# Kernel tuning notes

Hardware: AMD Instinct MI355X
Metric: run time of the kernel (lower is better)

Reference implementation:

```python
import jax, jax.numpy as jnp
import numpy as np

NUM_CLASSES = 20
NUM_ANCHORS = 3
STRIDES = (8, 16, 32)
FMP = (320, 160, 80)
TOPK = 100
CONF_THRESH = 0.01
NMS_THRESH = 0.5
ANCHOR_SIZE = np.array([[12, 16], [19, 36], [40, 28], [36, 75], [76, 55], [72, 146],
                        [142, 110], [192, 243], [459, 401]], dtype=np.float32).reshape(3, NUM_ANCHORS, 2)


def make_anchors(level):
    h = w = FMP[level]
    ys, xs = jnp.meshgrid(jnp.arange(h, dtype=jnp.float32), jnp.arange(w, dtype=jnp.float32), indexing='ij')
    xy = jnp.stack([xs, ys], axis=-1).reshape(-1, 1, 2) + 0.5            # [HW,1,2] grid centers
    xy = jnp.broadcast_to(xy, (h * w, NUM_ANCHORS, 2))
    wh = jnp.broadcast_to(jnp.asarray(ANCHOR_SIZE[level]), (h * w, NUM_ANCHORS, 2))
    return jnp.concatenate([xy, wh], axis=-1).reshape(-1, 4)             # [HW*A, 4]


def level_topk(obj, cls, reg, level):
    C = NUM_CLASSES
    # [1, ch, H, W] -> [H*W*A, ch_per_anchor], matching permute(1,2,0).view(-1, .)
    obj = obj[0].transpose(1, 2, 0).reshape(-1, 1)
    cls = cls[0].transpose(1, 2, 0).reshape(-1, C)
    reg = reg[0].transpose(1, 2, 0).reshape(-1, 4)
    anchors = make_anchors(level)
    # decode: ctr = (sigmoid(txy)*3 - 1.5 + grid) * stride ; wh = exp(twh) * anchor_wh
    ctr = (jax.nn.sigmoid(reg[:, :2]) * 3.0 - 1.5 + anchors[:, :2]) * STRIDES[level]
    wh = jnp.exp(reg[:, 2:]) * anchors[:, 2:]
    boxes = jnp.concatenate([ctr - 0.5 * wh, ctr + 0.5 * wh], axis=-1)   # [N, 4] xyxy
    scores = (jax.nn.sigmoid(obj) * jax.nn.sigmoid(cls)).reshape(-1)     # [N*C]
    top_s, top_i = jax.lax.top_k(scores, TOPK)
    anchor_idx = top_i // C
    labels = top_i % C
    return top_s, labels, boxes[anchor_idx], top_s > CONF_THRESH


def nms_fixed(boxes, scores, labels, valid):
    # class-aware greedy NMS on a fixed candidate set; suppressed entries get score 0 / keep False
    K = scores.shape[0]
    order = jnp.argsort(-scores)
    b, s, l, v = boxes[order], scores[order], labels[order], valid[order]
    areas = (b[:, 2] - b[:, 0]) * (b[:, 3] - b[:, 1])
    xx1 = jnp.maximum(b[:, None, 0], b[None, :, 0])
    yy1 = jnp.maximum(b[:, None, 1], b[None, :, 1])
    xx2 = jnp.minimum(b[:, None, 2], b[None, :, 2])
    yy2 = jnp.minimum(b[:, None, 3], b[None, :, 3])
    inter = jnp.maximum(1e-10, xx2 - xx1) * jnp.maximum(1e-10, yy2 - yy1)
    iou = inter / (areas[:, None] + areas[None, :] - inter)
    sup_mat = (iou > NMS_THRESH) & (l[:, None] == l[None, :])            # per-class suppression
    idx = jnp.arange(K)

    def body(i, state):
        suppressed, keep = state
        is_kept = jnp.logical_and(jnp.logical_not(suppressed[i]), v[i])
        keep = keep.at[i].set(is_kept)
        suppressed = suppressed | (is_kept & sup_mat[i] & (idx > i))
        return suppressed, keep

    _, keep = jax.lax.fori_loop(0, K, body, (jnp.zeros(K, bool), jnp.zeros(K, bool)))
    return b, s * keep.astype(s.dtype), l, keep


def setup_inputs() -> dict:
    key = jax.random.key(0)
    ks = jax.random.split(key, 9)
    shapes = {
        'obj0': (1, NUM_ANCHORS, 320, 320), 'cls0': (1, NUM_ANCHORS * NUM_CLASSES, 320, 320), 'reg0': (1, NUM_ANCHORS * 4, 320, 320),
        'obj1': (1, NUM_ANCHORS, 160, 160), 'cls1': (1, NUM_ANCHORS * NUM_CLASSES, 160, 160), 'reg1': (1, NUM_ANCHORS * 4, 160, 160),
        'obj2': (1, NUM_ANCHORS, 80, 80), 'cls2': (1, NUM_ANCHORS * NUM_CLASSES, 80, 80), 'reg2': (1, NUM_ANCHORS * 4, 80, 80),
    }
    return {name: jax.random.normal(k, shp, dtype=jnp.float32)
            for k, (name, shp) in zip(ks, shapes.items())}


def reference(obj0, cls0, reg0, obj1, cls1, reg1, obj2, cls2, reg2):
    levels = [(obj0, cls0, reg0), (obj1, cls1, reg1), (obj2, cls2, reg2)]
    parts = [level_topk(o, c, r, i) for i, (o, c, r) in enumerate(levels)]
    scores = jnp.concatenate([p[0] for p in parts])
    labels = jnp.concatenate([p[1] for p in parts])
    boxes = jnp.concatenate([p[2] for p in parts])
    valid = jnp.concatenate([p[3] for p in parts])
    return nms_fixed(boxes, scores, labels, valid)  # (bboxes[300,4], scores[300], labels[300], keep[300])
```

## Files before the change

### kernel.cpp

```cpp
#include <hip/hip_runtime.h>
#include <stdint.h>

typedef unsigned int u32;
typedef unsigned long long u64;

#define TOPK 100
#define CAP 4096
#define NB 512
#define BINBASE 32000u
#define KAB_BLOCKS 394

__device__ const float ANC[3][3][2] = {
  {{12.f,16.f},{19.f,36.f},{40.f,28.f}},
  {{36.f,75.f},{76.f,55.f},{72.f,146.f}},
  {{142.f,110.f},{192.f,243.f},{459.f,401.f}}
};

__device__ __forceinline__ float sigmoidf_(float x) {
  if (x >= 0.f) return 1.f / (1.f + expf(-x));
  float e = expf(x);
  return e / (1.f + e);
}

__device__ __forceinline__ float fcomp(const float4& v, int q) {
  switch (q) {
    case 0: return v.x;
    case 1: return v.y;
    case 2: return v.z;
    default: return v.w;
  }
}

__global__ __launch_bounds__(256) void kA_scan(
    const float* __restrict__ obj0, const float* __restrict__ cls0,
    const float* __restrict__ obj1, const float* __restrict__ cls1,
    const float* __restrict__ obj2, const float* __restrict__ cls2,
    u32* __restrict__ hist, float* __restrict__ amax)
{
  __shared__ u32 h[NB];
  int tid = threadIdx.x;
  h[tid] = 0; h[tid + 256] = 0;
  __syncthreads();

  int b = blockIdx.x;
  const float *obj, *cls; int P, L, abase; u32 task;
  if (b < 300)      { L=0; obj=obj0; cls=cls0; P=102400; abase=0;      task=(u32)(b*256+tid); }
  else if (b < 375) { L=1; obj=obj1; cls=cls1; P=25600;  abase=307200; task=(u32)((b-300)*256+tid); }
  else              { L=2; obj=obj2; cls=cls2; P=6400;   abase=384000; task=(u32)((b-375)*256+tid); }
  int tpa = P >> 2;
  bool valid = task < (u32)(3*tpa);

  if (valid) {
    int a = (int)(task / (u32)tpa), rem = (int)(task % (u32)tpa);
    int p0 = rem * 4;
    float4 o4 = *(const float4*)(obj + a*P + p0);
    const float* cp = cls + (size_t)(a*20)*P + p0;
    float4 cv[20];
    #pragma unroll
    for (int k = 0; k < 20; ++k) cv[k] = *(const float4*)(cp + (size_t)k*P);
    float4 cm = cv[0];
    #pragma unroll
    for (int k = 1; k < 20; ++k) {
      cm.x = fmaxf(cm.x, cv[k].x); cm.y = fmaxf(cm.y, cv[k].y);
      cm.z = fmaxf(cm.z, cv[k].z); cm.w = fmaxf(cm.w, cv[k].w);
    }
    float4 am4;
    am4.x = sigmoidf_(o4.x) * sigmoidf_(cm.x);
    am4.y = sigmoidf_(o4.y) * sigmoidf_(cm.y);
    am4.z = sigmoidf_(o4.z) * sigmoidf_(cm.z);
    am4.w = sigmoidf_(o4.w) * sigmoidf_(cm.w);
    *(float4*)(amax + abase + a*P + p0) = am4;
    #pragma unroll
    for (int q = 0; q < 4; ++q) {
      u32 bt = __float_as_uint(fcomp(am4, q));
      if (bt >= (BINBASE << 15)) {
        u32 bin = (bt >> 15) - BINBASE;
        if (bin < NB) atomicAdd(&h[bin], 1u);
      }
    }
  }
  __syncthreads();
  if (h[tid])       atomicAdd(&hist[L*NB + tid],       h[tid]);
  if (h[tid + 256]) atomicAdd(&hist[L*NB + tid + 256], h[tid + 256]);
}

__global__ __launch_bounds__(256) void kB_collect(
    const float* __restrict__ obj0, const float* __restrict__ cls0,
    const float* __restrict__ obj1, const float* __restrict__ cls1,
    const float* __restrict__ obj2, const float* __restrict__ cls2,
    const float* __restrict__ amax, const u32* __restrict__ hist,
    u32* __restrict__ cnt, u64* __restrict__ cand)
{
  __shared__ u32 s[NB];
  __shared__ u32 sThr;
  int tid = threadIdx.x;
  int b = blockIdx.x;
  const float *obj, *cls; int P, L, abase; u32 task;
  if (b < 300)      { L=0; obj=obj0; cls=cls0; P=102400; abase=0;      task=(u32)(b*256+tid); }
  else if (b < 375) { L=1; obj=obj1; cls=cls1; P=25600;  abase=307200; task=(u32)((b-300)*256+tid); }
  else              { L=2; obj=obj2; cls=cls2; P=6400;   abase=384000; task=(u32)((b-375)*256+tid); }
  int tpa = P >> 2;
  bool valid = task < (u32)(3*tpa);

  s[tid] = hist[L*NB + tid]; s[tid + 256] = hist[L*NB + tid + 256];
  __syncthreads();
  for (int off = 1; off < NB; off <<= 1) {
    u32 v0 = s[tid]       + ((tid + off < NB)       ? s[tid + off]       : 0u);
    u32 v1 = s[tid + 256] + ((tid + 256 + off < NB) ? s[tid + 256 + off] : 0u);
    __syncthreads();
    s[tid] = v0; s[tid + 256] = v1;
    __syncthreads();
  }
  if (tid == 0 && s[0] < TOPK) sThr = BINBASE << 15;
  {
    int i0 = tid, i1 = tid + 256;
    u32 a0 = s[i0], n0 = (i0 + 1 < NB) ? s[i0 + 1] : 0u;
    if (a0 >= TOPK && n0 < TOPK) sThr = (BINBASE + (u32)i0) << 15;
    u32 a1 = s[i1], n1 = (i1 + 1 < NB) ? s[i1 + 1] : 0u;
    if (a1 >= TOPK && n1 < TOPK) sThr = (BINBASE + (u32)i1) << 15;
  }
  __syncthreads();
  u32 thr = sThr;

  if (valid) {
    int a = (int)(task / (u32)tpa), rem = (int)(task % (u32)tpa);
    int p0 = rem * 4;
    float4 am4 = *(const float4*)(amax + abase + a*P + p0);
    bool any = (__float_as_uint(am4.x) >= thr) | (__float_as_uint(am4.y) >= thr) |
               (__float_as_uint(am4.z) >= thr) | (__float_as_uint(am4.w) >= thr);
    if (any) {
      float4 o4 = *(const float4*)(obj + a*P + p0);
      const float* cp = cls + (size_t)(a*20)*P + p0;
      float4 cv[20];
      #pragma unroll
      for (int k = 0; k < 20; ++k) cv[k] = *(const float4*)(cp + (size_t)k*P);
      #pragma unroll
      for (int q = 0; q < 4; ++q) {
        if (__float_as_uint(fcomp(am4, q)) >= thr) {
          float so = sigmoidf_(fcomp(o4, q));
          int p = p0 + q;
          #pragma unroll
          for (int k = 0; k < 20; ++k) {
            float sc = so * sigmoidf_(fcomp(cv[k], q));
            u32 bits = __float_as_uint(sc);
            if (bits >= thr) {
              u32 pos = atomicAdd(&cnt[L], 1u);
              u32 idx = (u32)(p*60 + a*20 + k);
              if (pos < CAP) cand[L*CAP + pos] = ((u64)bits << 32) | (u64)(0x00FFFFFFu - idx);
            }
          }
        }
      }
    }
  }
}

__global__ __launch_bounds__(1024) void kC_select_nms(
    const float* __restrict__ reg0, const float* __restrict__ reg1, const float* __restrict__ reg2,
    const u64* __restrict__ cand, const u32* __restrict__ cnt,
    float* __restrict__ out)
{
  extern __shared__ uint8_t smem[];
  u64*    keys  = (u64*)(smem);
  u64*    mat   = (u64*)(smem);
  float4* ibox4 = (float4*)(smem + 12000);
  float2* iml2  = (float2*)(smem + 16800);
  float*  x1s   = (float*)(smem + 19200);
  float*  y1s   = (float*)(smem + 20400);
  float*  x2s   = (float*)(smem + 21600);
  float*  y2s   = (float*)(smem + 22800);
  float*  sc2   = (float*)(smem + 24000);
  int*    lb2   = (int*)(smem + 25200);
  int*    vd2   = (int*)(smem + 26400);
  u64*    rowAny= (u64*)(smem + 27600);
  u64*    km    = (u64*)(smem + 27648);
  float*  ars   = (float*)(smem + 27696);
  u64*    sel   = (u64*)(smem + 32800);
  float*  bxs   = (float*)(smem + 35200);
  float*  scs   = (float*)(smem + 40000);
  int*    lbs   = (int*)(smem + 41200);
  int*    vds   = (int*)(smem + 42400);

  int tid = threadIdx.x;
  if (tid < 300) sel[tid] = 0ull;
  __syncthreads();

  for (int L = 0; L < 3; ++L) {
    u32 n = cnt[L]; if (n > CAP) n = CAP;
    u32 n4 = (n + 3u) & ~3u;
    for (u32 j = (u32)tid; j < n; j += 1024) keys[j] = cand[L*CAP + j];
    if (tid < 4 && n + (u32)tid < n4) keys[n + tid] = 0ull;
    __syncthreads();
    for (u32 j = (u32)tid; j < n; j += 1024) {
      u64 kk = keys[j]; int r = 0;
      for (u32 t = 0; t < n4; t += 4) {
        u64 k0 = keys[t], k1 = keys[t+1], k2 = keys[t+2], k3 = keys[t+3];
        r += (k0 > kk) ? 1 : 0; r += (k1 > kk) ? 1 : 0;
        r += (k2 > kk) ? 1 : 0; r += (k3 > kk) ? 1 : 0;
      }
      if (r < TOPK) sel[L*TOPK + r] = kk;
    }
    __syncthreads();
  }

  if (tid < 300) {
    int Lq = tid / TOPK;
    const float* reg; int Pq, W, stride;
    if (Lq == 0)      { reg = reg0; Pq = 102400; W = 320; stride = 8; }
    else if (Lq == 1) { reg = reg1; Pq = 25600;  W = 160; stride = 16; }
    else              { reg = reg2; Pq = 6400;   W = 80;  stride = 32; }
    u64 key = sel[tid];
    if (key == 0) {
      scs[tid] = 0.f; lbs[tid] = 0; vds[tid] = 0;
      bxs[tid*4+0] = bxs[tid*4+1] = bxs[tid*4+2] = bxs[tid*4+3] = 0.f;
    } else {
      float score = __uint_as_float((u32)(key >> 32));
      u32 i = 0x00FFFFFFu - (u32)(key & 0xFFFFFFFFull);
      int c = (int)(i % 60u), p = (int)(i / 60u);
      int aa = c / 20, k = c % 20;
      int x = p % W, y = p / W;
      float tx = reg[(aa*4+0)*Pq + p], ty = reg[(aa*4+1)*Pq + p];
      float tw = reg[(aa*4+2)*Pq + p], th = reg[(aa*4+3)*Pq + p];
      float cx = (sigmoidf_(tx)*3.f - 1.5f + (float)x + 0.5f) * (float)stride;
      float cy = (sigmoidf_(ty)*3.f - 1.5f + (float)y + 0.5f) * (float)stride;
      float bw = expf(tw) * ANC[Lq][aa][0];
      float bh = expf(th) * ANC[Lq][aa][1];
      scs[tid] = score; lbs[tid] = k; vds[tid] = (score > 0.01f) ? 1 : 0;
      bxs[tid*4+0] = cx - 0.5f*bw; bxs[tid*4+1] = cy - 0.5f*bh;
      bxs[tid*4+2] = cx + 0.5f*bw; bxs[tid*4+3] = cy + 0.5f*bh;
    }
  }
  __syncthreads();

  if (tid < 300) {
    int Lm = tid / TOPK, rr = tid % TOPK;
    u64 kk = sel[tid];
    int rank = rr;
    #pragma unroll
    for (int Lo = 0; Lo < 3; ++Lo) {
      if (Lo == Lm) continue;
      const u64* arr = sel + Lo*TOPK;
      bool ge = (Lo < Lm);
      int lo = 0;
      #pragma unroll
      for (int st = 64; st > 0; st >>= 1) {
        int nxt = lo + st;
        if (nxt <= TOPK) {
          u64 v = arr[nxt - 1];
          bool pred = ge ? (v >= kk) : (v > kk);
          if (pred) lo = nxt;
        }
      }
      rank += lo;
    }
    float x1 = bxs[tid*4+0], y1 = bxs[tid*4+1], x2 = bxs[tid*4+2], y2 = bxs[tid*4+3];
    float ar = (x2 - x1) * (y2 - y1);
    ibox4[rank] = make_float4(x1, y1, x2, y2);
    iml2[rank]  = make_float2(ar, (float)lbs[tid]);
    x1s[rank] = x1; y1s[rank] = y1; x2s[rank] = x2; y2s[rank] = y2; ars[rank] = ar;
    sc2[rank] = scs[tid]; lb2[rank] = lbs[tid]; vd2[rank] = vds[tid];
  }
  __syncthreads();

  {
    int wave = tid >> 6, lane = tid & 63;
    if (wave < 15) {
      int w = wave / 3, stripe = wave % 3;
      int j = w*64 + lane;
      bool jv = j < 300;
      float jx1=0.f, jy1=0.f, jx2=0.f, jy2=0.f, jar=0.f; float jlb=-1.f;
      if (jv) { jx1=x1s[j]; jy1=y1s[j]; jx2=x2s[j]; jy2=y2s[j]; jar=ars[j]; jlb=(float)lb2[j]; }
      int ilim = (w+1)*64; if (ilim > 300) ilim = 300;
      #pragma unroll 2
      for (int i = stripe; i < ilim; i += 3) {
        float4 B = ibox4[i];
        float2 M = iml2[i];
        float xx1 = fmaxf(B.x, jx1), yy1 = fmaxf(B.y, jy1);
        float xx2 = fminf(B.z, jx2), yy2 = fminf(B.w, jy2);
        float inter = fmaxf(1e-10f, xx2-xx1) * fmaxf(1e-10f, yy2-yy1);
        float iou = inter / (M.x + jar - inter);
        bool pred = jv && (iou > 0.5f) && (M.y == jlb);
        u64 m = __ballot(pred);
        if (lane == 0) mat[i*5 + w] = m;
      }
    }
  }
  __syncthreads();

  {
    bool flag = false;
    if (tid < 300) {
      int c = tid >> 6, bq = tid & 63;
      u64 acc = mat[tid*5 + c] & ((bq == 63) ? 0ull : (~0ull << (bq + 1)));
      for (int w = c + 1; w < 5; ++w) acc |= mat[tid*5 + w];
      flag = (acc != 0ull);
    }
    u64 bal = __ballot(flag);
    if ((tid & 63) == 0 && (tid >> 6) < 5) rowAny[tid >> 6] = bal;
  }
  __syncthreads();

  if (tid < 64) {
    int lane = tid;
    u64 vm[5];
    #pragma unroll
    for (int c = 0; c < 5; ++c) {
      int j = c*64 + lane;
      vm[c] = __ballot((j < 300) && (vd2[j] != 0));
    }
    u64 ra[5];
    #pragma unroll
    for (int c = 0; c < 5; ++c) ra[c] = rowAny[c];
    u64 S[5] = {0,0,0,0,0};
    #pragma unroll
    for (int c = 0; c < 5; ++c) {
      u64 kbits = 0;
      int lim = (c == 4) ? 44 : 64;
      for (int t = 0; t < lim; ++t) {
        u64 kept = ((~(S[c] >> t)) & (vm[c] >> t)) & 1ull;
        kbits |= kept << t;
        if (kept & ((ra[c] >> t) & 1ull)) {
          int i = c*64 + t;
          #pragma unroll
          for (int w = 0; w < 5; ++w)
            if (w >= c) S[w] |= mat[i*5 + w];
        }
      }
      if (lane == 0) km[c] = kbits;
    }
  }
  __syncthreads();

  if (tid < 300) {
    float kf = (float)((km[tid >> 6] >> (tid & 63)) & 1ull);
    float4 bq = ibox4[tid];
    out[tid*4+0] = bq.x; out[tid*4+1] = bq.y;
    out[tid*4+2] = bq.z; out[tid*4+3] = bq.w;
    out[1200+tid] = sc2[tid] * kf;
    out[1500+tid] = (float)lb2[tid];
    out[1800+tid] = kf;
  }
}

extern "C" void kernel_launch(void* const* d_in, const int* in_sizes, int n_in,
                              void* d_out, int out_size, void* d_ws, size_t ws_size,
                              hipStream_t stream) {
  const float* obj0 = (const float*)d_in[0];
  const float* cls0 = (const float*)d_in[1];
  const float* reg0 = (const float*)d_in[2];
  const float* obj1 = (const float*)d_in[3];
  const float* cls1 = (const float*)d_in[4];
  const float* reg1 = (const float*)d_in[5];
  const float* obj2 = (const float*)d_in[6];
  const float* cls2 = (const float*)d_in[7];
  const float* reg2 = (const float*)d_in[8];
  float* out = (float*)d_out;

  uint8_t* ws = (uint8_t*)d_ws;
  u32*   hist = (u32*)(ws + 0);
  u32*   cnt  = (u32*)(ws + 6144);
  u64*   cand = (u64*)(ws + 8192);
  float* amax = (float*)(ws + 106496);

  (void)hipMemsetAsync(ws, 0, 6160, stream);

  kA_scan<<<dim3(KAB_BLOCKS), dim3(256), 0, stream>>>(
      obj0, cls0, obj1, cls1, obj2, cls2, hist, amax);
  kB_collect<<<dim3(KAB_BLOCKS), dim3(256), 0, stream>>>(
      obj0, cls0, obj1, cls1, obj2, cls2, amax, hist, cnt, cand);
  kC_select_nms<<<dim3(1), dim3(1024), 46080, stream>>>(reg0, reg1, reg2, cand, cnt, out);
}
```

Baseline: 165.1 us.

## Split select+NMS kernel into per-level parallel select and separate NMS kernel

The single-block select+NMS kernel is split in two. The first kernel runs one block per pyramid level, doing the rank-based top-100 selection and box decode in parallel across levels and writing the results to workspace. The second kernel merges the levels and runs NMS. The IoU matrix build also changes from a uniform 3 stripes per column wave to a triangular split, giving later column groups more waves. This adds a kernel launch, a global round trip, and workspace reuse of the amax region, which is safe only if amax is dead by then.

```diff
diff --git a/kernel.cpp b/kernel.cpp
--- a/kernel.cpp
+++ b/kernel.cpp
@@ -155,13 +155,73 @@
   }
 }
 
-__global__ __launch_bounds__(1024) void kC_select_nms(
+__global__ __launch_bounds__(256) void kC1_select(
     const float* __restrict__ reg0, const float* __restrict__ reg1, const float* __restrict__ reg2,
     const u64* __restrict__ cand, const u32* __restrict__ cnt,
+    u64* __restrict__ selg, float* __restrict__ boxg, float* __restrict__ scg,
+    int* __restrict__ lbg, int* __restrict__ vdg)
+{
+  __shared__ u64 keys[CAP + 4];
+  __shared__ u64 selL[TOPK];
+  int tid = threadIdx.x;
+  int L = blockIdx.x;
+
+  if (tid < TOPK) selL[tid] = 0ull;
+  __syncthreads();
+
+  u32 n = cnt[L]; if (n > CAP) n = CAP;
+  u32 n4 = (n + 3u) & ~3u;
+  for (u32 j = (u32)tid; j < n; j += 256) keys[j] = cand[L*CAP + j];
+  if (tid < 4 && n + (u32)tid < n4) keys[n + tid] = 0ull;
+  __syncthreads();
+
+  for (u32 j = (u32)tid; j < n; j += 256) {
+    u64 kk = keys[j]; int r = 0;
+    for (u32 t = 0; t < n4; t += 4) {
+      u64 k0 = keys[t], k1 = keys[t+1], k2 = keys[t+2], k3 = keys[t+3];
+      r += (k0 > kk) ? 1 : 0; r += (k1 > kk) ? 1 : 0;
+      r += (k2 > kk) ? 1 : 0; r += (k3 > kk) ? 1 : 0;
+    }
+    if (r < TOPK) selL[r] = kk;
+  }
+  __syncthreads();
+
+  if (tid < TOPK) {
+    const float* reg; int Pq, W, stride;
+    if (L == 0)      { reg = reg0; Pq = 102400; W = 320; stride = 8; }
+    else if (L == 1) { reg = reg1; Pq = 25600;  W = 160; stride = 16; }
+    else             { reg = reg2; Pq = 6400;   W = 80;  stride = 32; }
+    int g = L*TOPK + tid;
+    u64 key = selL[tid];
+    selg[g] = key;
+    if (key == 0) {
+      scg[g] = 0.f; lbg[g] = 0; vdg[g] = 0;
+      boxg[g*4+0] = boxg[g*4+1] = boxg[g*4+2] = boxg[g*4+3] = 0.f;
+    } else {
+      float score = __uint_as_float((u32)(key >> 32));
+      u32 i = 0x00FFFFFFu - (u32)(key & 0xFFFFFFFFull);
+      int c = (int)(i % 60u), p = (int)(i / 60u);
+      int aa = c / 20, k = c % 20;
+      int x = p % W, y = p / W;
+      float tx = reg[(aa*4+0)*Pq + p], ty = reg[(aa*4+1)*Pq + p];
+      float tw = reg[(aa*4+2)*Pq + p], th = reg[(aa*4+3)*Pq + p];
+      float cx = (sigmoidf_(tx)*3.f - 1.5f + (float)x + 0.5f) * (float)stride;
+      float cy = (sigmoidf_(ty)*3.f - 1.5f + (float)y + 0.5f) * (float)stride;
+      float bw = expf(tw) * ANC[L][aa][0];
+      float bh = expf(th) * ANC[L][aa][1];
+      scg[g] = score; lbg[g] = k; vdg[g] = (score > 0.01f) ? 1 : 0;
+      boxg[g*4+0] = cx - 0.5f*bw; boxg[g*4+1] = cy - 0.5f*bh;
+      boxg[g*4+2] = cx + 0.5f*bw; boxg[g*4+3] = cy + 0.5f*bh;
+    }
+  }
+}
+
+__global__ __launch_bounds__(1024) void kC2_nms(
+    const u64* __restrict__ selg, const float* __restrict__ boxg,
+    const float* __restrict__ scg, const int* __restrict__ lbg, const int* __restrict__ vdg,
     float* __restrict__ out)
 {
   extern __shared__ uint8_t smem[];
-  u64*    keys  = (u64*)(smem);
   u64*    mat   = (u64*)(smem);
   float4* ibox4 = (float4*)(smem + 12000);
   float2* iml2  = (float2*)(smem + 16800);
@@ -175,71 +235,20 @@
   u64*    rowAny= (u64*)(smem + 27600);
   u64*    km    = (u64*)(smem + 27648);
   float*  ars   = (float*)(smem + 27696);
-  u64*    sel   = (u64*)(smem + 32800);
-  float*  bxs   = (float*)(smem + 35200);
-  float*  scs   = (float*)(smem + 40000);
-  int*    lbs   = (int*)(smem + 41200);
-  int*    vds   = (int*)(smem + 42400);
+  u64*    selAll= (u64*)(smem + 28896);
 
   int tid = threadIdx.x;
-  if (tid < 300) sel[tid] = 0ull;
-  __syncthreads();
-
-  for (int L = 0; L < 3; ++L) {
-    u32 n = cnt[L]; if (n > CAP) n = CAP;
-    u32 n4 = (n + 3u) & ~3u;
-    for (u32 j = (u32)tid; j < n; j += 1024) keys[j] = cand[L*CAP + j];
-    if (tid < 4 && n + (u32)tid < n4) keys[n + tid] = 0ull;
-    __syncthreads();
-    for (u32 j = (u32)tid; j < n; j += 1024) {
-      u64 kk = keys[j]; int r = 0;
-      for (u32 t = 0; t < n4; t += 4) {
-        u64 k0 = keys[t], k1 = keys[t+1], k2 = keys[t+2], k3 = keys[t+3];
-        r += (k0 > kk) ? 1 : 0; r += (k1 > kk) ? 1 : 0;
-        r += (k2 > kk) ? 1 : 0; r += (k3 > kk) ? 1 : 0;
-      }
-      if (r < TOPK) sel[L*TOPK + r] = kk;
-    }
-    __syncthreads();
-  }
-
-  if (tid < 300) {
-    int Lq = tid / TOPK;
-    const float* reg; int Pq, W, stride;
-    if (Lq == 0)      { reg = reg0; Pq = 102400; W = 320; stride = 8; }
-    else if (Lq == 1) { reg = reg1; Pq = 25600;  W = 160; stride = 16; }
-    else              { reg = reg2; Pq = 6400;   W = 80;  stride = 32; }
-    u64 key = sel[tid];
-    if (key == 0) {
-      scs[tid] = 0.f; lbs[tid] = 0; vds[tid] = 0;
-      bxs[tid*4+0] = bxs[tid*4+1] = bxs[tid*4+2] = bxs[tid*4+3] = 0.f;
-    } else {
-      float score = __uint_as_float((u32)(key >> 32));
-      u32 i = 0x00FFFFFFu - (u32)(key & 0xFFFFFFFFull);
-      int c = (int)(i % 60u), p = (int)(i / 60u);
-      int aa = c / 20, k = c % 20;
-      int x = p % W, y = p / W;
-      float tx = reg[(aa*4+0)*Pq + p], ty = reg[(aa*4+1)*Pq + p];
-      float tw = reg[(aa*4+2)*Pq + p], th = reg[(aa*4+3)*Pq + p];
-      float cx = (sigmoidf_(tx)*3.f - 1.5f + (float)x + 0.5f) * (float)stride;
-      float cy = (sigmoidf_(ty)*3.f - 1.5f + (float)y + 0.5f) * (float)stride;
-      float bw = expf(tw) * ANC[Lq][aa][0];
-      float bh = expf(th) * ANC[Lq][aa][1];
-      scs[tid] = score; lbs[tid] = k; vds[tid] = (score > 0.01f) ? 1 : 0;
-      bxs[tid*4+0] = cx - 0.5f*bw; bxs[tid*4+1] = cy - 0.5f*bh;
-      bxs[tid*4+2] = cx + 0.5f*bw; bxs[tid*4+3] = cy + 0.5f*bh;
-    }
-  }
+  if (tid < 300) selAll[tid] = selg[tid];
   __syncthreads();
 
   if (tid < 300) {
     int Lm = tid / TOPK, rr = tid % TOPK;
-    u64 kk = sel[tid];
+    u64 kk = selAll[tid];
     int rank = rr;
     #pragma unroll
     for (int Lo = 0; Lo < 3; ++Lo) {
       if (Lo == Lm) continue;
-      const u64* arr = sel + Lo*TOPK;
+      const u64* arr = selAll + Lo*TOPK;
       bool ge = (Lo < Lm);
       int lo = 0;
       #pragma unroll
@@ -253,26 +262,29 @@
       }
       rank += lo;
     }
-    float x1 = bxs[tid*4+0], y1 = bxs[tid*4+1], x2 = bxs[tid*4+2], y2 = bxs[tid*4+3];
+    float4 bb = *(const float4*)(boxg + tid*4);
+    float x1 = bb.x, y1 = bb.y, x2 = bb.z, y2 = bb.w;
     float ar = (x2 - x1) * (y2 - y1);
     ibox4[rank] = make_float4(x1, y1, x2, y2);
-    iml2[rank]  = make_float2(ar, (float)lbs[tid]);
+    iml2[rank]  = make_float2(ar, (float)lbg[tid]);
     x1s[rank] = x1; y1s[rank] = y1; x2s[rank] = x2; y2s[rank] = y2; ars[rank] = ar;
-    sc2[rank] = scs[tid]; lb2[rank] = lbs[tid]; vd2[rank] = vds[tid];
+    sc2[rank] = scg[tid]; lb2[rank] = lbg[tid]; vd2[rank] = vdg[tid];
   }
   __syncthreads();
 
   {
     int wave = tid >> 6, lane = tid & 63;
     if (wave < 15) {
-      int w = wave / 3, stripe = wave % 3;
+      int w = (wave >= 10) ? 4 : (wave >= 6) ? 3 : (wave >= 3) ? 2 : (wave >= 1) ? 1 : 0;
+      int ns = w + 1;
+      int stripe = wave - ((w*(w+1)) >> 1);
       int j = w*64 + lane;
       bool jv = j < 300;
       float jx1=0.f, jy1=0.f, jx2=0.f, jy2=0.f, jar=0.f; float jlb=-1.f;
       if (jv) { jx1=x1s[j]; jy1=y1s[j]; jx2=x2s[j]; jy2=y2s[j]; jar=ars[j]; jlb=(float)lb2[j]; }
       int ilim = (w+1)*64; if (ilim > 300) ilim = 300;
       #pragma unroll 2
-      for (int i = stripe; i < ilim; i += 3) {
+      for (int i = stripe; i < ilim; i += ns) {
         float4 B = ibox4[i];
         float2 M = iml2[i];
         float xx1 = fmaxf(B.x, jx1), yy1 = fmaxf(B.y, jy1);
@@ -361,6 +373,11 @@
   u32*   cnt  = (u32*)(ws + 6144);
   u64*   cand = (u64*)(ws + 8192);
   float* amax = (float*)(ws + 106496);
+  u64*   selg = (u64*)(ws + 106496);
+  float* boxg = (float*)(ws + 108896);
+  float* scg  = (float*)(ws + 113696);
+  int*   lbg  = (int*)(ws + 114896);
+  int*   vdg  = (int*)(ws + 116096);
 
   (void)hipMemsetAsync(ws, 0, 6160, stream);
 
@@ -368,5 +385,8 @@
       obj0, cls0, obj1, cls1, obj2, cls2, hist, amax);
   kB_collect<<<dim3(KAB_BLOCKS), dim3(256), 0, stream>>>(
       obj0, cls0, obj1, cls1, obj2, cls2, amax, hist, cnt, cand);
-  kC_select_nms<<<dim3(1), dim3(1024), 46080, stream>>>(reg0, reg1, reg2, cand, cnt, out);
-}
+  kC1_select<<<dim3(3), dim3(256), 0, stream>>>(
+      reg0, reg1, reg2, cand, cnt, selg, boxg, scg, lbg, vdg);
+  kC2_nms<<<dim3(1), dim3(1024), 31744, stream>>>(
+      selg, boxg, scg, lbg, vdg, out);
+}
```

Result: faster. 157.3 us (-4.7%).

## Halve per-thread work in scan kernels, parallelize per-level selection, rebalance IoU waves

Applied to the files above, without the earlier changes.

The scan and collect kernels now process two pixels per thread using float2 loads, which doubles the block count to 788 and raises parallelism and memory-level concurrency across the GPU. The single-block select/NMS kernel now ranks candidates for all three levels at once, each with its own thread group, instead of looping over levels in sequence. Keys are kept in LDS when a level has few candidates, and a global-memory fallback handles larger counts. The IoU matrix waves are split in proportion to the triangular workload per column block, and the shared-memory size is reduced. The costs are narrower loads per thread, fewer threads working on each level's ranking, and a slow global-memory path if a level's candidate count is large.

```diff
diff --git a/kernel.cpp b/kernel.cpp
--- a/kernel.cpp
+++ b/kernel.cpp
@@ -8,7 +8,7 @@
 #define CAP 4096
 #define NB 512
 #define BINBASE 32000u
-#define KAB_BLOCKS 394
+#define KAB_BLOCKS 788
 
 __device__ const float ANC[3][3][2] = {
   {{12.f,16.f},{19.f,36.f},{40.f,28.f}},
@@ -22,13 +22,8 @@
   return e / (1.f + e);
 }
 
-__device__ __forceinline__ float fcomp(const float4& v, int q) {
-  switch (q) {
-    case 0: return v.x;
-    case 1: return v.y;
-    case 2: return v.z;
-    default: return v.w;
-  }
+__device__ __forceinline__ float fcomp2(const float2& v, int q) {
+  return q ? v.y : v.x;
 }
 
 __global__ __launch_bounds__(256) void kA_scan(
@@ -44,35 +39,32 @@
 
   int b = blockIdx.x;
   const float *obj, *cls; int P, L, abase; u32 task;
-  if (b < 300)      { L=0; obj=obj0; cls=cls0; P=102400; abase=0;      task=(u32)(b*256+tid); }
-  else if (b < 375) { L=1; obj=obj1; cls=cls1; P=25600;  abase=307200; task=(u32)((b-300)*256+tid); }
-  else              { L=2; obj=obj2; cls=cls2; P=6400;   abase=384000; task=(u32)((b-375)*256+tid); }
-  int tpa = P >> 2;
+  if (b < 600)      { L=0; obj=obj0; cls=cls0; P=102400; abase=0;      task=(u32)(b*256+tid); }
+  else if (b < 750) { L=1; obj=obj1; cls=cls1; P=25600;  abase=307200; task=(u32)((b-600)*256+tid); }
+  else              { L=2; obj=obj2; cls=cls2; P=6400;   abase=384000; task=(u32)((b-750)*256+tid); }
+  int tpa = P >> 1;
   bool valid = task < (u32)(3*tpa);
 
   if (valid) {
     int a = (int)(task / (u32)tpa), rem = (int)(task % (u32)tpa);
-    int p0 = rem * 4;
-    float4 o4 = *(const float4*)(obj + a*P + p0);
+    int p0 = rem * 2;
+    float2 o2 = *(const float2*)(obj + a*P + p0);
     const float* cp = cls + (size_t)(a*20)*P + p0;
-    float4 cv[20];
-    #pragma unroll
-    for (int k = 0; k < 20; ++k) cv[k] = *(const float4*)(cp + (size_t)k*P);
-    float4 cm = cv[0];
+    float2 cv[20];
+    #pragma unroll
+    for (int k = 0; k < 20; ++k) cv[k] = *(const float2*)(cp + (size_t)k*P);
+    float2 cm = cv[0];
     #pragma unroll
     for (int k = 1; k < 20; ++k) {
       cm.x = fmaxf(cm.x, cv[k].x); cm.y = fmaxf(cm.y, cv[k].y);
-      cm.z = fmaxf(cm.z, cv[k].z); cm.w = fmaxf(cm.w, cv[k].w);
-    }
-    float4 am4;
-    am4.x = sigmoidf_(o4.x) * sigmoidf_(cm.x);
-    am4.y = sigmoidf_(o4.y) * sigmoidf_(cm.y);
-    am4.z = sigmoidf_(o4.z) * sigmoidf_(cm.z);
-    am4.w = sigmoidf_(o4.w) * sigmoidf_(cm.w);
-    *(float4*)(amax + abase + a*P + p0) = am4;
-    #pragma unroll
-    for (int q = 0; q < 4; ++q) {
-      u32 bt = __float_as_uint(fcomp(am4, q));
+    }
+    float2 am2;
+    am2.x = sigmoidf_(o2.x) * sigmoidf_(cm.x);
+    am2.y = sigmoidf_(o2.y) * sigmoidf_(cm.y);
+    *(float2*)(amax + abase + a*P + p0) = am2;
+    #pragma unroll
+    for (int q = 0; q < 2; ++q) {
+      u32 bt = __float_as_uint(fcomp2(am2, q));
       if (bt >= (BINBASE << 15)) {
         u32 bin = (bt >> 15) - BINBASE;
         if (bin < NB) atomicAdd(&h[bin], 1u);
@@ -96,10 +88,10 @@
   int tid = threadIdx.x;
   int b = blockIdx.x;
   const float *obj, *cls; int P, L, abase; u32 task;
-  if (b < 300)      { L=0; obj=obj0; cls=cls0; P=102400; abase=0;      task=(u32)(b*256+tid); }
-  else if (b < 375) { L=1; obj=obj1; cls=cls1; P=25600;  abase=307200; task=(u32)((b-300)*256+tid); }
-  else              { L=2; obj=obj2; cls=cls2; P=6400;   abase=384000; task=(u32)((b-375)*256+tid); }
-  int tpa = P >> 2;
+  if (b < 600)      { L=0; obj=obj0; cls=cls0; P=102400; abase=0;      task=(u32)(b*256+tid); }
+  else if (b < 750) { L=1; obj=obj1; cls=cls1; P=25600;  abase=307200; task=(u32)((b-600)*256+tid); }
+  else              { L=2; obj=obj2; cls=cls2; P=6400;   abase=384000; task=(u32)((b-750)*256+tid); }
+  int tpa = P >> 1;
   bool valid = task < (u32)(3*tpa);
 
   s[tid] = hist[L*NB + tid]; s[tid + 256] = hist[L*NB + tid + 256];
@@ -124,24 +116,23 @@
 
   if (valid) {
     int a = (int)(task / (u32)tpa), rem = (int)(task % (u32)tpa);
-    int p0 = rem * 4;
-    float4 am4 = *(const float4*)(amax + abase + a*P + p0);
-    bool any = (__float_as_uint(am4.x) >= thr) | (__float_as_uint(am4.y) >= thr) |
-               (__float_as_uint(am4.z) >= thr) | (__float_as_uint(am4.w) >= thr);
+    int p0 = rem * 2;
+    float2 am2 = *(const float2*)(amax + abase + a*P + p0);
+    bool any = (__float_as_uint(am2.x) >= thr) | (__float_as_uint(am2.y) >= thr);
     if (any) {
-      float4 o4 = *(const float4*)(obj + a*P + p0);
+      float2 o2 = *(const float2*)(obj + a*P + p0);
       const float* cp = cls + (size_t)(a*20)*P + p0;
-      float4 cv[20];
+      float2 cv[20];
       #pragma unroll
-      for (int k = 0; k < 20; ++k) cv[k] = *(const float4*)(cp + (size_t)k*P);
+      for (int k = 0; k < 20; ++k) cv[k] = *(const float2*)(cp + (size_t)k*P);
       #pragma unroll
-      for (int q = 0; q < 4; ++q) {
-        if (__float_as_uint(fcomp(am4, q)) >= thr) {
-          float so = sigmoidf_(fcomp(o4, q));
+      for (int q = 0; q < 2; ++q) {
+        if (__float_as_uint(fcomp2(am2, q)) >= thr) {
+          float so = sigmoidf_(fcomp2(o2, q));
           int p = p0 + q;
           #pragma unroll
           for (int k = 0; k < 20; ++k) {
-            float sc = so * sigmoidf_(fcomp(cv[k], q));
+            float sc = so * sigmoidf_(fcomp2(cv[k], q));
             u32 bits = __float_as_uint(sc);
             if (bits >= thr) {
               u32 pos = atomicAdd(&cnt[L], 1u);
@@ -161,7 +152,6 @@
     float* __restrict__ out)
 {
   extern __shared__ uint8_t smem[];
-  u64*    keys  = (u64*)(smem);
   u64*    mat   = (u64*)(smem);
   float4* ibox4 = (float4*)(smem + 12000);
   float2* iml2  = (float2*)(smem + 16800);
@@ -185,23 +175,48 @@
   if (tid < 300) sel[tid] = 0ull;
   __syncthreads();
 
-  for (int L = 0; L < 3; ++L) {
-    u32 n = cnt[L]; if (n > CAP) n = CAP;
+  {
+    int gL    = (tid >= 768) ? 2 : (tid >= 384) ? 1 : 0;
+    int gbase = (gL == 2) ? 768 : (gL == 1) ? 384 : 0;
+    int lt    = tid - gbase;
+    int gsz   = (gL == 2) ? 256 : 384;
+
+    u32 n = cnt[gL]; if (n > CAP) n = CAP;
+    bool useLds = (n <= 496);
+    u64* kc = mat + gL*500;
+    const u64* cb = cand + gL*CAP;
     u32 n4 = (n + 3u) & ~3u;
-    for (u32 j = (u32)tid; j < n; j += 1024) keys[j] = cand[L*CAP + j];
-    if (tid < 4 && n + (u32)tid < n4) keys[n + tid] = 0ull;
+
+    if (useLds) {
+      for (u32 j = (u32)lt; j < n; j += gsz) kc[j] = cb[j];
+      if (lt < 4 && n + (u32)lt < n4) kc[n + lt] = 0ull;
+    }
     __syncthreads();
-    for (u32 j = (u32)tid; j < n; j += 1024) {
-      u64 kk = keys[j]; int r = 0;
-      for (u32 t = 0; t < n4; t += 4) {
-        u64 k0 = keys[t], k1 = keys[t+1], k2 = keys[t+2], k3 = keys[t+3];
-        r += (k0 > kk) ? 1 : 0; r += (k1 > kk) ? 1 : 0;
-        r += (k2 > kk) ? 1 : 0; r += (k3 > kk) ? 1 : 0;
-      }
-      if (r < TOPK) sel[L*TOPK + r] = kk;
-    }
-    __syncthreads();
-  }
+
+    if (useLds) {
+      for (u32 j = (u32)lt; j < n; j += gsz) {
+        u64 kk = kc[j]; int r = 0;
+        for (u32 t = 0; t < n4; t += 4) {
+          u64 k0 = kc[t], k1 = kc[t+1], k2 = kc[t+2], k3 = kc[t+3];
+          r += (k0 > kk) ? 1 : 0; r += (k1 > kk) ? 1 : 0;
+          r += (k2 > kk) ? 1 : 0; r += (k3 > kk) ? 1 : 0;
+        }
+        if (r < TOPK) sel[gL*TOPK + r] = kk;
+      }
+    } else {
+      u32 nn = n & ~3u;
+      for (u32 j = (u32)lt; j < n; j += gsz) {
+        u64 kk = cb[j]; int r = 0;
+        for (u32 t = 0; t < nn; t += 4) {
+          r += (cb[t]   > kk) ? 1 : 0; r += (cb[t+1] > kk) ? 1 : 0;
+          r += (cb[t+2] > kk) ? 1 : 0; r += (cb[t+3] > kk) ? 1 : 0;
+        }
+        for (u32 t = nn; t < n; ++t) r += (cb[t] > kk) ? 1 : 0;
+        if (r < TOPK) sel[gL*TOPK + r] = kk;
+      }
+    }
+  }
+  __syncthreads();
 
   if (tid < 300) {
     int Lq = tid / TOPK;
@@ -265,14 +280,16 @@
   {
     int wave = tid >> 6, lane = tid & 63;
     if (wave < 15) {
-      int w = wave / 3, stripe = wave % 3;
+      int w = (wave >= 10) ? 4 : (wave >= 6) ? 3 : (wave >= 3) ? 2 : (wave >= 1) ? 1 : 0;
+      int ns = w + 1;
+      int stripe = wave - ((w*(w+1)) >> 1);
       int j = w*64 + lane;
       bool jv = j < 300;
       float jx1=0.f, jy1=0.f, jx2=0.f, jy2=0.f, jar=0.f; float jlb=-1.f;
       if (jv) { jx1=x1s[j]; jy1=y1s[j]; jx2=x2s[j]; jy2=y2s[j]; jar=ars[j]; jlb=(float)lb2[j]; }
       int ilim = (w+1)*64; if (ilim > 300) ilim = 300;
       #pragma unroll 2
-      for (int i = stripe; i < ilim; i += 3) {
+      for (int i = stripe; i < ilim; i += ns) {
         float4 B = ibox4[i];
         float2 M = iml2[i];
         float xx1 = fmaxf(B.x, jx1), yy1 = fmaxf(B.y, jy1);
@@ -368,5 +385,5 @@
       obj0, cls0, obj1, cls1, obj2, cls2, hist, amax);
   kB_collect<<<dim3(KAB_BLOCKS), dim3(256), 0, stream>>>(
       obj0, cls0, obj1, cls1, obj2, cls2, amax, hist, cnt, cand);
-  kC_select_nms<<<dim3(1), dim3(1024), 46080, stream>>>(reg0, reg1, reg2, cand, cnt, out);
-}
+  kC_select_nms<<<dim3(1), dim3(1024), 43600, stream>>>(reg0, reg1, reg2, cand, cnt, out);
+}
```

Measured after the change: 155.7 us. 1.06x faster.
